# Optimization experiments

Measured on AMD Instinct MI355X. Metric: run time of the kernel, lower is better.

Reference implementation:

```python
import jax, jax.numpy as jnp
import numpy as np

N_NODES = 20000
N_EDGES = 320000
N_GRAPHS = 200
N_LAYERS = 2
TOWERS = 5
F_IN = 75        # divide_input=False -> each tower sees the full 75-dim input
F_OUT = 15       # out_channels // towers = 75 // 5
EDGE_DIM = 50
POST_IN = (4 * 3 + 1) * F_IN  # 4 aggregators * 3 scalers + self = 975
EPS_STD = 1e-5
EPS_BN = 1e-5


def setup_inputs() -> dict:
    key = jax.random.key(0)
    ks = jax.random.split(key, 16)
    x_idx = jax.random.randint(ks[0], (N_NODES,), 0, 10000)
    edge_index = jax.random.randint(ks[1], (2, N_EDGES), 0, N_NODES)
    edge_attr_idx = jax.random.randint(ks[2], (N_EDGES,), 0, 100)
    batch_idx = jnp.sort(jax.random.randint(ks[3], (N_NODES,), 0, N_GRAPHS))

    def g(k, shp, fan):
        return jax.random.normal(k, shp, jnp.float32) * np.float32(1.0 / np.sqrt(fan))

    inp = dict(
        x_idx=x_idx, edge_index=edge_index, edge_attr_idx=edge_attr_idx, batch_idx=batch_idx,
        node_emb=g(ks[4], (10000, F_IN), 1.0),
        edge_emb=g(ks[5], (100, EDGE_DIM), 1.0),
        W_edge=g(ks[6], (N_LAYERS, EDGE_DIM, F_IN), EDGE_DIM),
        b_edge=jnp.zeros((N_LAYERS, F_IN), jnp.float32),
        W_pre=g(ks[7], (N_LAYERS, TOWERS, 3 * F_IN, F_IN), 3 * F_IN),
        b_pre=jnp.zeros((N_LAYERS, TOWERS, F_IN), jnp.float32),
        W_post=g(ks[8], (N_LAYERS, TOWERS, POST_IN, F_OUT), POST_IN),
        b_post=jnp.zeros((N_LAYERS, TOWERS, F_OUT), jnp.float32),
        W_lin=g(ks[9], (N_LAYERS, F_IN, F_IN), F_IN),
        b_lin=jnp.zeros((N_LAYERS, F_IN), jnp.float32),
        bn_gamma=jnp.ones((N_LAYERS, F_IN), jnp.float32),
        bn_beta=jnp.zeros((N_LAYERS, F_IN), jnp.float32),
        W1=g(ks[10], (75, 50), 75), b1=jnp.zeros((50,), jnp.float32),
        W2=g(ks[11], (50, 25), 50), b2=jnp.zeros((25,), jnp.float32),
        W3=g(ks[12], (25, 1), 25), b3=jnp.zeros((1,), jnp.float32),
    )
    return inp


def reference(x_idx, edge_index, edge_attr_idx, batch_idx,
              node_emb, edge_emb, W_edge, b_edge, W_pre, b_pre,
              W_post, b_post, W_lin, b_lin, bn_gamma, bn_beta,
              W1, b1, W2, b2, W3, b3):
    src, dst = edge_index[0], edge_index[1]  # flow source_to_target: aggregate at dst
    x = node_emb[x_idx]                      # [N, 75]
    e_raw = edge_emb[edge_attr_idx]          # [E, 50]

    # in-degree based scalers (PNA); avg log-degree from this graph's degree histogram
    deg = jax.ops.segment_sum(jnp.ones((N_EDGES,), jnp.float32), dst, num_segments=N_NODES)
    avg_log = jnp.mean(jnp.log(deg + 1.0))
    deg_c = jnp.maximum(deg, 1.0)
    amp = (jnp.log(deg_c + 1.0) / avg_log)[:, None, None]
    att = (avg_log / jnp.log(deg_c + 1.0))[:, None, None]
    has_in = (deg > 0.0)[:, None, None]
    inv_deg = (1.0 / deg_c)[:, None, None]

    for l in range(N_LAYERS):
        # edge encoder (shared across towers)
        e = e_raw @ W_edge[l] + b_edge[l]                            # [E, 75]
        # message: since divide_input=False all towers see the same concat input
        h = jnp.concatenate([x[dst], x[src], e], axis=-1)            # [E, 225]
        m = jnp.einsum('ec,tcf->etf', h, W_pre[l]) + b_pre[l]        # [E, T, 75]
        # multi-aggregator reduction at dst
        mean = jax.ops.segment_sum(m, dst, num_segments=N_NODES) * inv_deg
        mean_sq = jax.ops.segment_sum(m * m, dst, num_segments=N_NODES) * inv_deg
        std = jnp.sqrt(jax.nn.relu(mean_sq - mean * mean) + EPS_STD)
        mn = jnp.where(has_in, jax.ops.segment_min(m, dst, num_segments=N_NODES), 0.0)
        mx = jnp.where(has_in, jax.ops.segment_max(m, dst, num_segments=N_NODES), 0.0)
        aggr = jnp.concatenate([mean, mn, mx, std], axis=-1)         # [N, T, 300]
        # degree scalers: identity, amplification, attenuation
        out = jnp.concatenate([aggr, aggr * amp, aggr * att], axis=-1)  # [N, T, 900]
        # update: concat self features, per-tower post MLP, then shared lin
        xt = jnp.broadcast_to(x[:, None, :], (N_NODES, TOWERS, F_IN))
        h2 = jnp.concatenate([xt, out], axis=-1)                     # [N, T, 975]
        y = jnp.einsum('ntc,tcf->ntf', h2, W_post[l]) + b_post[l]    # [N, T, 15]
        y = y.reshape(N_NODES, TOWERS * F_OUT) @ W_lin[l] + b_lin[l] # [N, 75]
        # BatchNorm (training-mode batch stats, biased variance) + ReLU
        mu = jnp.mean(y, axis=0)
        var = jnp.mean((y - mu) ** 2, axis=0)
        y = (y - mu) * jax.lax.rsqrt(var + EPS_BN) * bn_gamma[l] + bn_beta[l]
        x = jax.nn.relu(y)

    pooled = jax.ops.segment_sum(x, batch_idx, num_segments=N_GRAPHS)  # [G, 75]
    h = jax.nn.relu(pooled @ W1 + b1)
    h = jax.nn.relu(h @ W2 + b2)
    return h @ W3 + b3                                               # [G, 1]
```

## Files before the change

kernel.cpp:

```cpp
#include <hip/hip_runtime.h>
#include <hip/hip_bf16.h>
#include <math.h>

#define NN 20000
#define NE 320000
#define NG 200
#define FI 75
#define NT 5
#define FO 15
#define CH 375
#define PI 975
#define SMS 1608

typedef __attribute__((ext_vector_type(8))) short v8s;
typedef __attribute__((ext_vector_type(4))) float v4f;

__device__ __forceinline__ unsigned short f2bfu(float v) {
  __hip_bfloat16 h = __float2bfloat16(v);
  return *reinterpret_cast<unsigned short*>(&h);
}
__device__ __forceinline__ float uif(unsigned u) { return __uint_as_float(u); }

__global__ __launch_bounds__(256) void k_mega1(
    const int* __restrict__ xidx, const float* __restrict__ emb, float* __restrict__ x,
    const int* __restrict__ dstp, int* __restrict__ deg,
    const float* __restrict__ eemb, const float* __restrict__ W_edge,
    const float* __restrict__ b_edge, float* __restrict__ te,
    const float* __restrict__ W_pre, float* __restrict__ WAs,
    const float* __restrict__ W_post, float* __restrict__ V,
    const float* __restrict__ b_post, const float* __restrict__ W_lin,
    const float* __restrict__ b_lin, float* __restrict__ bc) {
  __shared__ float S[FI * 16];
  int b = blockIdx.x, tid = threadIdx.x;
  if (b < 5860) {
    int i = b * 256 + tid;
    if (i < NN * FI) {
      int n = i / FI, f = i - n * FI;
      x[i] = emb[xidx[n] * FI + f];
    }
  } else if (b < 7110) {
    int e = (b - 5860) * 256 + tid;
    if (e < NE) atomicAdd(&deg[dstp[e]], 1);
  } else if (b < 7310) {
    int la = b - 7110;
    int l = la / 100, a = la - l * 100;
    int f = tid;
    if (f < FI) {
      float acc = b_edge[l * FI + f];
      for (int j = 0; j < 50; ++j)
        acc = fmaf(eemb[a * 50 + j], W_edge[(l * 50 + j) * FI + f], acc);
      te[la * FI + f] = acc;
    }
  } else if (b < 7530) {
    int i = (b - 7310) * 256 + tid;
    if (i < 2 * FI * CH) {
      int c = i % CH;
      int k = (i / CH) % FI;
      int l = i / (CH * FI);
      int t = c / FI, f = c - t * FI;
      WAs[i] = W_pre[((size_t)(l * NT + t) * 225 + FI + k) * FI + f];
    }
  } else if (b < 7560) {
    int bid = b - 7530;
    int g = bid % 3;
    int lt = bid / 3;
    for (int idx = tid; idx < FI * 16; idx += 256) {
      int q = idx >> 4, f = idx & 15;
      float v = 0.f;
      if (f < FO) {
        const float* wb = W_post + (size_t)lt * PI * FO;
        int rowb = FI + g * 300 + q;
        v = wb[rowb * FO + f] + wb[(rowb + FI) * FO + f] + wb[(rowb + 2 * FI) * FO + f];
      }
      S[idx] = v;
    }
    __syncthreads();
    for (int idx = tid; idx < FI * 16; idx += 256) {
      int j = idx >> 4, f = idx & 15;
      float acc = 0.f;
      const float* wr = W_pre + ((size_t)lt * 225 + j) * FI;
      for (int q = 0; q < FI; ++q) acc = fmaf(wr[q], S[q * 16 + f], acc);
      V[((size_t)bid * FI + j) * 16 + f] = acc;
    }
  } else {
    int l = b - 7560;
    int g = tid;
    if (g < FI) {
      float acc = b_lin[l * FI + g];
      for (int j = 0; j < FI; ++j)
        acc = fmaf(b_post[l * FI + j], W_lin[(l * FI + j) * FI + g], acc);
      bc[l * 76 + g] = acc;
    }
  }
}

__global__ __launch_bounds__(1024) void k_mega2(
    const int* __restrict__ deg, int* __restrict__ off, int* __restrict__ cur,
    float* __restrict__ avglog,
    const float* __restrict__ te, const float* __restrict__ W_pre,
    const float* __restrict__ b_pre, unsigned short* __restrict__ tm,
    const float* __restrict__ W_post, const float* __restrict__ V,
    unsigned short* __restrict__ Bp,
    const float* __restrict__ WAs, unsigned short* __restrict__ Bxs,
    const float* __restrict__ W_lin, unsigned short* __restrict__ Blin) {
  __shared__ float red[1024];
  int b = blockIdx.x, t = threadIdx.x;
  if (b == 0) {
    int* wsum = (int*)red;
    int base = t * 20;
    int loc[20];
    int s = 0;
#pragma unroll
    for (int j = 0; j < 20; ++j) {
      int i = base + j;
      int v = (i < NN) ? deg[i] : 0;
      loc[j] = s;
      s += v;
    }
    int lane = t & 63, w = t >> 6;
    int inc = s;
    for (int o = 1; o < 64; o <<= 1) {
      int u = __shfl_up(inc, o, 64);
      if (lane >= o) inc += u;
    }
    if (lane == 63) wsum[w] = inc;
    __syncthreads();
    if (t == 0) {
      int a = 0;
#pragma unroll
      for (int k = 0; k < 16; ++k) { int v = wsum[k]; wsum[k] = a; a += v; }
    }
    __syncthreads();
    int tex = wsum[w] + inc - s;
#pragma unroll
    for (int j = 0; j < 20; ++j) {
      int i = base + j;
      if (i < NN) { int e = tex + loc[j]; off[i] = e; cur[i] = e; }
    }
    if (t == 1023) off[NN] = tex + s;
  } else if (b == 1) {
    float s = 0.f;
    for (int i = t; i < NN; i += 1024) s += logf((float)deg[i] + 1.f);
    red[t] = s;
    __syncthreads();
    for (int o = 512; o > 0; o >>= 1) {
      if (t < o) red[t] += red[t + o];
      __syncthreads();
    }
    if (t == 0) avglog[0] = red[0] / (float)NN;
  } else if (b < 77) {
    int idx = (b - 2) * 1024 + t;
    if (idx < 76800) {
      int la = idx / 384, c = idx - la * 384;
      int l = la / 100;
      float acc = 0.f;
      if (c < CH) {
        int tt = c / FI, f = c - tt * FI;
        acc = b_pre[(l * NT + tt) * FI + f];
        const float* ter = te + la * FI;
        for (int k = 0; k < FI; ++k)
          acc = fmaf(ter[k], W_pre[((size_t)(l * NT + tt) * 225 + 150 + k) * FI + f], acc);
      }
      tm[(size_t)la * 384 + c] = f2bfu(acc);
    }
  } else if (b < 302) {
    int i = (b - 77) * 1024 + t;
    if (i < 230400) {
      int j = i & 7;
      int lane = (i >> 3) & 63;
      int rem = i >> 9;
      int kb = rem % 15; rem /= 15;
      int g = rem % 3; rem /= 3;
      int tt = rem % 5;
      int l = rem / 5;
      int k = kb * 32 + (lane >> 4) * 8 + j;
      int f = lane & 15;
      float w = 0.f;
      if (f < FO) {
        int lt = l * NT + tt;
        if (k < 300) {
          int a = k / 75, ch = k - a * 75;
          w = W_post[((size_t)lt * PI + FI + g * 300 + a * 75 + ch) * FO + f];
        } else if (k >= 320 && k < 395) {
          w = V[(((size_t)(lt * 3 + g)) * FI + (k - 320)) * 16 + f];
        } else if (k >= 395 && k < 470 && g == 0) {
          w = W_post[((size_t)lt * PI + (k - 395)) * FO + f];
        }
      }
      Bp[i] = f2bfu(w);
    }
  } else if (b < 374) {
    int i = (b - 302) * 1024 + t;
    if (i < 73728) {
      int j = i & 7;
      int lane = (i >> 3) & 63;
      int rem = i >> 9;
      int nt = rem % 24; rem /= 24;
      int kb = rem % 3;
      int l = rem / 3;
      int k = kb * 32 + (lane >> 4) * 8 + j;
      int n = nt * 16 + (lane & 15);
      float w = 0.f;
      if (k < FI && n < CH) w = WAs[(size_t)l * FI * CH + k * CH + n];
      Bxs[i] = f2bfu(w);
    }
  } else {
    int i = (b - 374) * 1024 + t;
    if (i < 15360) {
      int j = i & 7;
      int lane = (i >> 3) & 63;
      int rem = i >> 9;
      int nt = rem % 5; rem /= 5;
      int kb = rem % 3;
      int l = rem / 3;
      int k = kb * 32 + (lane >> 4) * 8 + j;
      int f = nt * 16 + (lane & 15);
      float w = 0.f;
      if (k < FI && f < FI) w = W_lin[(size_t)l * FI * FI + k * FI + f];
      Blin[i] = f2bfu(w);
    }
  }
}

__global__ __launch_bounds__(256) void k_mega3(
    const int* __restrict__ srcp, const int* __restrict__ dstp,
    const int* __restrict__ attr, int* __restrict__ cur, int2* __restrict__ csr,
    const int* __restrict__ deg, const float* __restrict__ avglog,
    float* __restrict__ amp, float* __restrict__ att, float* __restrict__ inv) {
  int b = blockIdx.x, t = threadIdx.x;
  if (b < 1250) {
    int e = b * 256 + t;
    if (e < NE) {
      int pos = atomicAdd(&cur[dstp[e]], 1);
      csr[pos] = make_int2(srcp[e], attr[e]);
    }
  } else {
    int i = (b - 1250) * 256 + t;
    if (i < NN) {
      float dc = fmaxf((float)deg[i], 1.f);
      float ld = logf(dc + 1.f);
      float av = avglog[0];
      amp[i] = ld / av;
      att[i] = av / ld;
      inv[i] = 1.f / dc;
    }
  }
}

__global__ __launch_bounds__(256) void k_gemm_xs(const float* __restrict__ x,
                                                 const unsigned short* __restrict__ BxsL,
                                                 unsigned short* __restrict__ xsb,
                                                 const int* __restrict__ deg,
                                                 unsigned short* __restrict__ xh,
                                                 float* __restrict__ bnsum) {
  int tid = threadIdx.x;
  if (blockIdx.y == 1) {
    if (blockIdx.x == 0 && tid < 150) bnsum[tid] = 0.f;
    for (int i = blockIdx.x * 256 + tid; i < NN * 160; i += 625 * 256) {
      int r = i / 160, k = i - r * 160;
      float v = 0.f;
      if (k < FI) v = x[(size_t)r * FI + k] * ((deg[r] > 0) ? 1.f : 0.f);
      else if (k < 150) v = x[(size_t)r * FI + k - FI];
      xh[i] = f2bfu(v);
    }
    return;
  }
  __shared__ unsigned short As[32 * 104];
  __shared__ unsigned short Os[32 * 384];
  int m0 = blockIdx.x * 32;
  for (int i = tid; i < 32 * 104; i += 256) {
    int r = i / 104, k = i - r * 104;
    As[i] = (k < FI) ? f2bfu(x[(size_t)(m0 + r) * FI + k]) : 0;
  }
  __syncthreads();
  int lane = tid & 63, w = tid >> 6;
  int m16 = lane & 15, quad = lane >> 4;
  v4f acc0[6], acc1[6];
#pragma unroll
  for (int nt = 0; nt < 6; ++nt) {
    acc0[nt] = {0.f, 0.f, 0.f, 0.f};
    acc1[nt] = {0.f, 0.f, 0.f, 0.f};
  }
  const unsigned short* arow0 = As + m16 * 104 + quad * 8;
  const unsigned short* arow1 = As + (16 + m16) * 104 + quad * 8;
#pragma unroll
  for (int kb = 0; kb < 3; ++kb) {
    v8s a0 = *(const v8s*)(arow0 + kb * 32);
    v8s a1 = *(const v8s*)(arow1 + kb * 32);
#pragma unroll
    for (int nt = 0; nt < 6; ++nt) {
      v8s bf = *(const v8s*)(BxsL + ((size_t)(kb * 24 + w * 6 + nt) * 64 + lane) * 8);
      acc0[nt] = __builtin_amdgcn_mfma_f32_16x16x32_bf16(a0, bf, acc0[nt], 0, 0, 0);
      acc1[nt] = __builtin_amdgcn_mfma_f32_16x16x32_bf16(a1, bf, acc1[nt], 0, 0, 0);
    }
  }
#pragma unroll
  for (int nt = 0; nt < 6; ++nt) {
    int col = w * 96 + nt * 16 + m16;
#pragma unroll
    for (int r = 0; r < 4; ++r) {
      Os[(quad * 4 + r) * 384 + col] = f2bfu(acc0[nt][r]);
      Os[(16 + quad * 4 + r) * 384 + col] = f2bfu(acc1[nt][r]);
    }
  }
  __syncthreads();
  uint4* dst = (uint4*)(xsb + (size_t)m0 * 384);
  const uint4* src = (const uint4*)Os;
  for (int i = tid; i < 1536; i += 256) dst[i] = src[i];
}

__global__ __launch_bounds__(1024) void k_aggpost(
    const unsigned short* __restrict__ xs, const int2* __restrict__ csr,
    const int* __restrict__ off, const float* __restrict__ inv_deg,
    const unsigned short* __restrict__ tm, const unsigned short* __restrict__ xh,
    const unsigned short* __restrict__ Bp, const float* __restrict__ amp,
    const float* __restrict__ att, const unsigned short* __restrict__ BlinL,
    const float* __restrict__ bcL, float* __restrict__ yout,
    float* __restrict__ bnsum) {
  __shared__ __align__(16) unsigned short sm[16 * SMS];
  __shared__ __align__(16) unsigned short zs[16 * 96];
  __shared__ float ysum[FI], ysq[FI];
  int tid = threadIdx.x;
  int wv = tid >> 6, lane = tid & 63;
  int rel0 = blockIdx.x * 16;
  int n = rel0 + wv;
  if (tid < FI) { ysum[tid] = 0.f; ysq[tid] = 0.f; }
  for (int idx = tid; idx < 1600; idx += 1024) {
    int h = idx / 100, pp = idx - h * 100;
    int t = pp / 20, cc = pp - t * 20;
    sm[h * SMS + t * 320 + 300 + cc] = 0;
  }
  for (int i = tid; i < 16 * 21; i += 1024) {
    int r = i / 21, k = 75 + i - r * 21;
    zs[r * 96 + k] = 0;
  }
  if (n < NN) {
    int c0 = lane * 6;
    int o0 = off[n], o1 = off[n + 1];
    float s[6], q[6], mn[6], mx[6];
#pragma unroll
    for (int j = 0; j < 6; ++j) {
      s[j] = 0.f; q[j] = 0.f; mn[j] = INFINITY; mx[j] = -INFINITY;
    }
    auto proc = [&](uint3 xv, uint3 tv) {
      unsigned xa[3] = {xv.x, xv.y, xv.z};
      unsigned ta[3] = {tv.x, tv.y, tv.z};
#pragma unroll
      for (int j = 0; j < 3; ++j) {
        float z0 = uif(xa[j] << 16) + uif(ta[j] << 16);
        float z1 = uif(xa[j] & 0xffff0000u) + uif(ta[j] & 0xffff0000u);
        s[2 * j] += z0; q[2 * j] = fmaf(z0, z0, q[2 * j]);
        mn[2 * j] = fminf(mn[2 * j], z0); mx[2 * j] = fmaxf(mx[2 * j], z0);
        s[2 * j + 1] += z1; q[2 * j + 1] = fmaf(z1, z1, q[2 * j + 1]);
        mn[2 * j + 1] = fminf(mn[2 * j + 1], z1); mx[2 * j + 1] = fmaxf(mx[2 * j + 1], z1);
      }
    };
    int i = o0;
    for (; i + 4 <= o1; i += 4) {
      int2 e0 = csr[i], e1 = csr[i + 1], e2 = csr[i + 2], e3 = csr[i + 3];
      uint3 x0 = *(const uint3*)(xs + (size_t)e0.x * 384 + c0);
      uint3 t0 = *(const uint3*)(tm + (size_t)e0.y * 384 + c0);
      uint3 x1 = *(const uint3*)(xs + (size_t)e1.x * 384 + c0);
      uint3 t1 = *(const uint3*)(tm + (size_t)e1.y * 384 + c0);
      uint3 x2 = *(const uint3*)(xs + (size_t)e2.x * 384 + c0);
      uint3 t2 = *(const uint3*)(tm + (size_t)e2.y * 384 + c0);
      uint3 x3 = *(const uint3*)(xs + (size_t)e3.x * 384 + c0);
      uint3 t3 = *(const uint3*)(tm + (size_t)e3.y * 384 + c0);
      proc(x0, t0); proc(x1, t1); proc(x2, t2); proc(x3, t3);
    }
    for (; i < o1; ++i) {
      int2 e0 = csr[i];
      uint3 x0 = *(const uint3*)(xs + (size_t)e0.x * 384 + c0);
      uint3 t0 = *(const uint3*)(tm + (size_t)e0.y * 384 + c0);
      proc(x0, t0);
    }
    float inv = inv_deg[n];
    bool empty = (o1 == o0);
    unsigned short* srow = sm + wv * SMS;
#pragma unroll
    for (int j = 0; j < 6; ++j) {
      int c = c0 + j;
      if (c < CH) {
        float me = s[j] * inv;
        float sd = sqrtf(fmaxf(q[j] * inv - me * me, 0.f) + 1e-5f);
        float mnv = empty ? 0.f : mn[j];
        float mxv = empty ? 0.f : mx[j];
        int t = c / 75, ch = c - t * 75;
        unsigned short* bb = srow + t * 320;
        bb[ch] = f2bfu(me);
        bb[75 + ch] = f2bfu(mnv);
        bb[150 + ch] = f2bfu(mxv);
        bb[225 + ch] = f2bfu(sd);
      }
    }
  } else {
    uint* rowz = (uint*)(sm + wv * SMS);
    for (int idx2 = lane; idx2 < SMS / 2; idx2 += 64) rowz[idx2] = 0;
  }
  __syncthreads();
  int m16 = lane & 15, quad = lane >> 4;
  if (wv < NT) {
    int tw = wv;
    const unsigned short* arow = sm + m16 * SMS + tw * 320 + quad * 8;
    const unsigned short* xrow = xh + (size_t)(rel0 + m16) * 160 + quad * 8;
    const unsigned short* bp = Bp + ((size_t)tw * 3 * 15 * 64) * 8 + lane * 8;
    v4f a0 = {0.f, 0.f, 0.f, 0.f}, a1 = a0, a2 = a0;
#pragma unroll
    for (int kb = 0; kb < 15; ++kb) {
      v8s av = *(const v8s*)((kb < 10) ? (arow + kb * 32) : (xrow + (kb - 10) * 32));
      const unsigned short* bb = bp + (size_t)kb * 512;
      v8s b0 = *(const v8s*)(bb);
      v8s b1 = *(const v8s*)(bb + 15 * 512);
      v8s b2 = *(const v8s*)(bb + 30 * 512);
      a0 = __builtin_amdgcn_mfma_f32_16x16x32_bf16(av, b0, a0, 0, 0, 0);
      a1 = __builtin_amdgcn_mfma_f32_16x16x32_bf16(av, b1, a1, 0, 0, 0);
      a2 = __builtin_amdgcn_mfma_f32_16x16x32_bf16(av, b2, a2, 0, 0, 0);
    }
    int f = m16;
    if (f < FO) {
      int relZ = quad * 4;
#pragma unroll
      for (int r = 0; r < 4; ++r) {
        int nd = rel0 + relZ + r;
        int ndc = (nd < NN) ? nd : (NN - 1);
        float zz = a0[r] + amp[ndc] * a1[r] + att[ndc] * a2[r];
        zs[(relZ + r) * 96 + tw * FO + f] = f2bfu(zz);
      }
    }
  }
  __syncthreads();
  if (wv < NT) {
    int tw = wv;
    v4f acc2 = {0.f, 0.f, 0.f, 0.f};
#pragma unroll
    for (int kb = 0; kb < 3; ++kb) {
      v8s av = *(const v8s*)(zs + m16 * 96 + quad * 8 + kb * 32);
      v8s bl = *(const v8s*)(BlinL + ((size_t)(kb * 5 + tw) * 64 + lane) * 8);
      acc2 = __builtin_amdgcn_mfma_f32_16x16x32_bf16(av, bl, acc2, 0, 0, 0);
    }
    int fcol = tw * 16 + m16;
    if (fcol < FI) {
      float bcf = bcL[fcol];
      int nb = rel0 + quad * 4;
#pragma unroll
      for (int r = 0; r < 4; ++r) {
        int nd = nb + r;
        if (nd < NN) {
          float v = acc2[r] + bcf;
          yout[(size_t)nd * FI + fcol] = v;
          atomicAdd(&ysum[fcol], v);
          atomicAdd(&ysq[fcol], v * v);
        }
      }
    }
  }
  __syncthreads();
  if (tid < FI) {
    atomicAdd(&bnsum[tid], ysum[tid]);
    atomicAdd(&bnsum[FI + tid], ysq[tid]);
  }
}

__global__ __launch_bounds__(256) void k_bnfinapply(const float* __restrict__ y,
    const float* __restrict__ bnsum, const float* __restrict__ gamL,
    const float* __restrict__ betL, float* __restrict__ xo,
    const int* __restrict__ batch, float* __restrict__ pooled, int dopool) {
  __shared__ float sc[150];
  int tid = threadIdx.x;
  if (tid < FI) {
    float mu = bnsum[tid] / (float)NN;
    float var = bnsum[FI + tid] / (float)NN - mu * mu;
    float scl = gamL[tid] * rsqrtf(var + 1e-5f);
    sc[tid] = scl;
    sc[FI + tid] = betL[tid] - mu * scl;
  }
  if (!dopool) {
    for (int i = blockIdx.x * 256 + tid; i < NG * FI; i += gridDim.x * 256)
      pooled[i] = 0.f;
  }
  __syncthreads();
  int stride = gridDim.x * 256;
  for (int i = blockIdx.x * 256 + tid; i < NN * FI; i += stride) {
    int n = i / FI, f = i - n * FI;
    float v = fmaxf(fmaf(y[i], sc[f], sc[FI + f]), 0.f);
    xo[i] = v;
    if (dopool) atomicAdd(&pooled[batch[n] * FI + f], v);
  }
}

__global__ void k_head(const float* __restrict__ pooled, const float* __restrict__ W1,
                       const float* __restrict__ b1, const float* __restrict__ W2,
                       const float* __restrict__ b2, const float* __restrict__ W3,
                       const float* __restrict__ b3, float* __restrict__ out) {
  __shared__ float p[FI], h1[50], h2[25];
  int g = blockIdx.x, t = threadIdx.x;
  for (int i = t; i < FI; i += 64) p[i] = pooled[g * FI + i];
  __syncthreads();
  if (t < 50) {
    float a = b1[t];
    for (int j = 0; j < FI; ++j) a = fmaf(p[j], W1[j * 50 + t], a);
    h1[t] = fmaxf(a, 0.f);
  }
  __syncthreads();
  if (t < 25) {
    float a = b2[t];
    for (int j = 0; j < 50; ++j) a = fmaf(h1[j], W2[j * 25 + t], a);
    h2[t] = fmaxf(a, 0.f);
  }
  __syncthreads();
  if (t == 0) {
    float a = b3[0];
    for (int j = 0; j < 25; ++j) a = fmaf(h2[j], W3[j], a);
    out[g] = a;
  }
}

extern "C" void kernel_launch(void* const* d_in, const int* in_sizes, int n_in,
                              void* d_out, int out_size, void* d_ws, size_t ws_size,
                              hipStream_t stream) {
  const int* x_idx = (const int*)d_in[0];
  const int* eidx  = (const int*)d_in[1];
  const int* srcp  = eidx;
  const int* dstp  = eidx + NE;
  const int* eattr = (const int*)d_in[2];
  const int* batch = (const int*)d_in[3];
  const float* node_emb = (const float*)d_in[4];
  const float* edge_emb = (const float*)d_in[5];
  const float* W_edge = (const float*)d_in[6];
  const float* b_edge = (const float*)d_in[7];
  const float* W_pre  = (const float*)d_in[8];
  const float* b_pre  = (const float*)d_in[9];
  const float* W_post = (const float*)d_in[10];
  const float* b_post = (const float*)d_in[11];
  const float* W_lin  = (const float*)d_in[12];
  const float* b_lin  = (const float*)d_in[13];
  const float* gam = (const float*)d_in[14];
  const float* bet = (const float*)d_in[15];
  const float* W1 = (const float*)d_in[16];
  const float* b1 = (const float*)d_in[17];
  const float* W2 = (const float*)d_in[18];
  const float* b2 = (const float*)d_in[19];
  const float* W3 = (const float*)d_in[20];
  const float* b3 = (const float*)d_in[21];

  char* p = (char*)d_ws;
  auto alloc = [&](size_t b) -> char* {
    char* r = p;
    p += (b + 255) & ~(size_t)255;
    return r;
  };
  float* x_a   = (float*)alloc((size_t)NN * FI * 4);
  float* x_b   = (float*)alloc((size_t)NN * FI * 4);
  unsigned short* xs_bf = (unsigned short*)alloc((size_t)NN * 384 * 2);
  float* z     = (float*)alloc((size_t)NN * FI * 4);
  unsigned short* xh = (unsigned short*)alloc((size_t)(NN + 64) * 160 * 2);
  float* te    = (float*)alloc(2 * 100 * FI * 4);
  unsigned short* tm_bf = (unsigned short*)alloc((size_t)2 * 100 * 384 * 2);
  float* WAs   = (float*)alloc((size_t)2 * FI * CH * 4);
  float* V     = (float*)alloc((size_t)2 * NT * 3 * FI * 16 * 4);
  unsigned short* Bpk = (unsigned short*)alloc((size_t)230400 * 2);
  unsigned short* Bxs = (unsigned short*)alloc((size_t)73728 * 2);
  unsigned short* Blin = (unsigned short*)alloc((size_t)15360 * 2);
  float* bc    = (float*)alloc(2 * 76 * 4);
  float* ampv  = (float*)alloc((size_t)NN * 4);
  float* attv  = (float*)alloc((size_t)NN * 4);
  float* invv  = (float*)alloc((size_t)NN * 4);
  float* avglog = (float*)alloc(256);
  float* bnsum = (float*)alloc(2 * FI * 4);
  float* pooled = (float*)alloc((size_t)NG * FI * 4);
  int* deg = (int*)alloc((size_t)NN * 4);
  int* off = (int*)alloc((size_t)(NN + 1) * 4);
  int* cur = (int*)alloc((size_t)NN * 4);
  int2* csr = (int2*)alloc((size_t)NE * 8);

  hipMemsetAsync(deg, 0, (size_t)NN * 4, stream);

  k_mega1<<<7562, 256, 0, stream>>>(x_idx, node_emb, x_a, dstp, deg,
                                    edge_emb, W_edge, b_edge, te,
                                    W_pre, WAs, W_post, V,
                                    b_post, W_lin, b_lin, bc);
  k_mega2<<<389, 1024, 0, stream>>>(deg, off, cur, avglog,
                                    te, W_pre, b_pre, tm_bf, W_post, V, Bpk,
                                    WAs, Bxs, W_lin, Blin);
  k_mega3<<<1329, 256, 0, stream>>>(srcp, dstp, eattr, cur, csr,
                                    deg, avglog, ampv, attv, invv);

  for (int l = 0; l < 2; ++l) {
    const float* xin = (l == 0) ? x_a : x_b;
    float* xout = (l == 0) ? x_b : x_a;
    k_gemm_xs<<<dim3(625, 2), 256, 0, stream>>>(xin, Bxs + (size_t)l * 36864,
                                                xs_bf, deg, xh, bnsum);
    k_aggpost<<<1250, 1024, 0, stream>>>(xs_bf, csr, off, invv,
                                         tm_bf + (size_t)l * 100 * 384, xh,
                                         Bpk + (size_t)l * 115200, ampv, attv,
                                         Blin + (size_t)l * 7680, bc + l * 76,
                                         z, bnsum);
    k_bnfinapply<<<1250, 256, 0, stream>>>(z, bnsum, gam + l * FI, bet + l * FI,
                                           xout, batch, pooled, (l == 1) ? 1 : 0);
  }

  k_head<<<NG, 64, 0, stream>>>(pooled, W1, b1, W2, b2, W3, b3, (float*)d_out);
}
```

Measured before the change: 433.1 us.

## Compute per-edge pre-MLP messages via MFMA inside aggregation instead of per-node precompute

Drops the per-node x·W_pre GEMM kernel and the precomputed per-edge-type term table. The aggregation kernel now gathers raw bf16 source features and edge-embedding rows into shared memory for each 32-edge tile, using a warp-specialized, double-buffered staging loop. It then runs MFMA over a stacked [x | te] K=160 weight to form the messages before reducing mean/min/max/std. This reads 160 bf16 per edge instead of 750 and removes one kernel, at the cost of more MFMA work per edge and a sync per tile.

```diff
diff --git a/kernel.cpp b/kernel.cpp
--- a/kernel.cpp
+++ b/kernel.cpp
@@ -97,11 +97,11 @@
 __global__ __launch_bounds__(1024) void k_mega2(
     const int* __restrict__ deg, int* __restrict__ off, int* __restrict__ cur,
     float* __restrict__ avglog,
-    const float* __restrict__ te, const float* __restrict__ W_pre,
-    const float* __restrict__ b_pre, unsigned short* __restrict__ tm,
+    const float* __restrict__ te, unsigned short* __restrict__ tq,
+    const float* __restrict__ W_pre,
     const float* __restrict__ W_post, const float* __restrict__ V,
     unsigned short* __restrict__ Bp,
-    const float* __restrict__ WAs, unsigned short* __restrict__ Bxs,
+    const float* __restrict__ WAs, unsigned short* __restrict__ Bx2,
     const float* __restrict__ W_lin, unsigned short* __restrict__ Blin) {
   __shared__ float red[1024];
   int b = blockIdx.x, t = threadIdx.x;
@@ -148,23 +148,36 @@
       __syncthreads();
     }
     if (t == 0) avglog[0] = red[0] / (float)NN;
-  } else if (b < 77) {
+  } else if (b < 18) {
     int idx = (b - 2) * 1024 + t;
-    if (idx < 76800) {
-      int la = idx / 384, c = idx - la * 384;
-      int l = la / 100;
-      float acc = 0.f;
-      if (c < CH) {
-        int tt = c / FI, f = c - tt * FI;
-        acc = b_pre[(l * NT + tt) * FI + f];
-        const float* ter = te + la * FI;
-        for (int k = 0; k < FI; ++k)
-          acc = fmaf(ter[k], W_pre[((size_t)(l * NT + tt) * 225 + 150 + k) * FI + f], acc);
+    if (idx < 16000) {
+      int la = idx / 80, k = idx - la * 80;
+      tq[idx] = (k < FI) ? f2bfu(te[la * FI + k]) : 0;
+    }
+  } else if (b < 138) {
+    int i = (b - 18) * 1024 + t;
+    if (i < 122880) {
+      int j = i & 7;
+      int lane = (i >> 3) & 63;
+      int rem = i >> 9;
+      int nt = rem % 24; rem /= 24;
+      int kb = rem % 5;
+      int l = rem / 5;
+      int k = kb * 32 + (lane >> 4) * 8 + j;
+      int n = nt * 16 + (lane & 15);
+      float w = 0.f;
+      if (n < CH) {
+        if (k < FI) {
+          w = WAs[(size_t)l * FI * CH + k * CH + n];
+        } else if (k >= 80 && k < 80 + FI) {
+          int tt = n / 75, f = n - tt * 75;
+          w = W_pre[((size_t)(l * NT + tt) * 225 + 150 + (k - 80)) * FI + f];
+        }
       }
-      tm[(size_t)la * 384 + c] = f2bfu(acc);
-    }
-  } else if (b < 302) {
-    int i = (b - 77) * 1024 + t;
+      Bx2[i] = f2bfu(w);
+    }
+  } else if (b < 363) {
+    int i = (b - 138) * 1024 + t;
     if (i < 230400) {
       int j = i & 7;
       int lane = (i >> 3) & 63;
@@ -189,23 +202,8 @@
       }
       Bp[i] = f2bfu(w);
     }
-  } else if (b < 374) {
-    int i = (b - 302) * 1024 + t;
-    if (i < 73728) {
-      int j = i & 7;
-      int lane = (i >> 3) & 63;
-      int rem = i >> 9;
-      int nt = rem % 24; rem /= 24;
-      int kb = rem % 3;
-      int l = rem / 3;
-      int k = kb * 32 + (lane >> 4) * 8 + j;
-      int n = nt * 16 + (lane & 15);
-      float w = 0.f;
-      if (k < FI && n < CH) w = WAs[(size_t)l * FI * CH + k * CH + n];
-      Bxs[i] = f2bfu(w);
-    }
   } else {
-    int i = (b - 374) * 1024 + t;
+    int i = (b - 363) * 1024 + t;
     if (i < 15360) {
       int j = i & 7;
       int lane = (i >> 3) & 63;
@@ -247,83 +245,46 @@
   }
 }
 
-__global__ __launch_bounds__(256) void k_gemm_xs(const float* __restrict__ x,
-                                                 const unsigned short* __restrict__ BxsL,
-                                                 unsigned short* __restrict__ xsb,
-                                                 const int* __restrict__ deg,
-                                                 unsigned short* __restrict__ xh,
-                                                 float* __restrict__ bnsum) {
+__global__ __launch_bounds__(256) void k_prepx(const float* __restrict__ x,
+                                               const int* __restrict__ deg,
+                                               unsigned short* __restrict__ xh,
+                                               unsigned short* __restrict__ xq,
+                                               float* __restrict__ bnsum) {
   int tid = threadIdx.x;
-  if (blockIdx.y == 1) {
-    if (blockIdx.x == 0 && tid < 150) bnsum[tid] = 0.f;
-    for (int i = blockIdx.x * 256 + tid; i < NN * 160; i += 625 * 256) {
-      int r = i / 160, k = i - r * 160;
-      float v = 0.f;
-      if (k < FI) v = x[(size_t)r * FI + k] * ((deg[r] > 0) ? 1.f : 0.f);
-      else if (k < 150) v = x[(size_t)r * FI + k - FI];
-      xh[i] = f2bfu(v);
-    }
-    return;
-  }
-  __shared__ unsigned short As[32 * 104];
-  __shared__ unsigned short Os[32 * 384];
-  int m0 = blockIdx.x * 32;
-  for (int i = tid; i < 32 * 104; i += 256) {
-    int r = i / 104, k = i - r * 104;
-    As[i] = (k < FI) ? f2bfu(x[(size_t)(m0 + r) * FI + k]) : 0;
-  }
-  __syncthreads();
-  int lane = tid & 63, w = tid >> 6;
-  int m16 = lane & 15, quad = lane >> 4;
-  v4f acc0[6], acc1[6];
-#pragma unroll
-  for (int nt = 0; nt < 6; ++nt) {
-    acc0[nt] = {0.f, 0.f, 0.f, 0.f};
-    acc1[nt] = {0.f, 0.f, 0.f, 0.f};
-  }
-  const unsigned short* arow0 = As + m16 * 104 + quad * 8;
-  const unsigned short* arow1 = As + (16 + m16) * 104 + quad * 8;
-#pragma unroll
-  for (int kb = 0; kb < 3; ++kb) {
-    v8s a0 = *(const v8s*)(arow0 + kb * 32);
-    v8s a1 = *(const v8s*)(arow1 + kb * 32);
-#pragma unroll
-    for (int nt = 0; nt < 6; ++nt) {
-      v8s bf = *(const v8s*)(BxsL + ((size_t)(kb * 24 + w * 6 + nt) * 64 + lane) * 8);
-      acc0[nt] = __builtin_amdgcn_mfma_f32_16x16x32_bf16(a0, bf, acc0[nt], 0, 0, 0);
-      acc1[nt] = __builtin_amdgcn_mfma_f32_16x16x32_bf16(a1, bf, acc1[nt], 0, 0, 0);
-    }
-  }
-#pragma unroll
-  for (int nt = 0; nt < 6; ++nt) {
-    int col = w * 96 + nt * 16 + m16;
-#pragma unroll
-    for (int r = 0; r < 4; ++r) {
-      Os[(quad * 4 + r) * 384 + col] = f2bfu(acc0[nt][r]);
-      Os[(16 + quad * 4 + r) * 384 + col] = f2bfu(acc1[nt][r]);
-    }
-  }
-  __syncthreads();
-  uint4* dst = (uint4*)(xsb + (size_t)m0 * 384);
-  const uint4* src = (const uint4*)Os;
-  for (int i = tid; i < 1536; i += 256) dst[i] = src[i];
+  if (blockIdx.x == 0 && tid < 150) bnsum[tid] = 0.f;
+  for (int i = blockIdx.x * 256 + tid; i < NN * 160; i += 625 * 256) {
+    int r = i / 160, k = i - r * 160;
+    float v = 0.f;
+    if (k < FI) v = x[(size_t)r * FI + k] * ((deg[r] > 0) ? 1.f : 0.f);
+    else if (k < 150) v = x[(size_t)r * FI + k - FI];
+    xh[i] = f2bfu(v);
+  }
+  for (int i = blockIdx.x * 256 + tid; i < NN * 80; i += 625 * 256) {
+    int r = i / 80, k = i - r * 80;
+    xq[i] = (k < FI) ? f2bfu(x[(size_t)r * FI + k]) : 0;
+  }
 }
 
 __global__ __launch_bounds__(1024) void k_aggpost(
-    const unsigned short* __restrict__ xs, const int2* __restrict__ csr,
-    const int* __restrict__ off, const float* __restrict__ inv_deg,
-    const unsigned short* __restrict__ tm, const unsigned short* __restrict__ xh,
+    const unsigned short* __restrict__ xq, const unsigned short* __restrict__ tqL,
+    const int2* __restrict__ csr, const int* __restrict__ off,
+    const float* __restrict__ inv_deg, const unsigned short* __restrict__ xh,
     const unsigned short* __restrict__ Bp, const float* __restrict__ amp,
     const float* __restrict__ att, const unsigned short* __restrict__ BlinL,
-    const float* __restrict__ bcL, float* __restrict__ yout,
-    float* __restrict__ bnsum) {
+    const float* __restrict__ bcL, const float* __restrict__ bpreL,
+    float* __restrict__ yout, float* __restrict__ bnsum,
+    const unsigned short* __restrict__ Bx2L) {
   __shared__ __align__(16) unsigned short sm[16 * SMS];
+  __shared__ __align__(16) unsigned short Ab[2][32 * 168];
   __shared__ __align__(16) unsigned short zs[16 * 96];
+  __shared__ int offL[17];
+  __shared__ int cumR[17];
   __shared__ float ysum[FI], ysq[FI];
   int tid = threadIdx.x;
   int wv = tid >> 6, lane = tid & 63;
+  int m16 = lane & 15, quad = lane >> 4;
   int rel0 = blockIdx.x * 16;
-  int n = rel0 + wv;
+  if (tid < 17) offL[tid] = off[rel0 + tid];
   if (tid < FI) { ysum[tid] = 0.f; ysq[tid] = 0.f; }
   for (int idx = tid; idx < 1600; idx += 1024) {
     int h = idx / 100, pp = idx - h * 100;
@@ -334,71 +295,165 @@
     int r = i / 21, k = 75 + i - r * 21;
     zs[r * 96 + k] = 0;
   }
-  if (n < NN) {
-    int c0 = lane * 6;
-    int o0 = off[n], o1 = off[n + 1];
-    float s[6], q[6], mn[6], mx[6];
-#pragma unroll
-    for (int j = 0; j < 6; ++j) {
-      s[j] = 0.f; q[j] = 0.f; mn[j] = INFINITY; mx[j] = -INFINITY;
-    }
-    auto proc = [&](uint3 xv, uint3 tv) {
-      unsigned xa[3] = {xv.x, xv.y, xv.z};
-      unsigned ta[3] = {tv.x, tv.y, tv.z};
-#pragma unroll
-      for (int j = 0; j < 3; ++j) {
-        float z0 = uif(xa[j] << 16) + uif(ta[j] << 16);
-        float z1 = uif(xa[j] & 0xffff0000u) + uif(ta[j] & 0xffff0000u);
-        s[2 * j] += z0; q[2 * j] = fmaf(z0, z0, q[2 * j]);
-        mn[2 * j] = fminf(mn[2 * j], z0); mx[2 * j] = fmaxf(mx[2 * j], z0);
-        s[2 * j + 1] += z1; q[2 * j + 1] = fmaf(z1, z1, q[2 * j + 1]);
-        mn[2 * j + 1] = fminf(mn[2 * j + 1], z1); mx[2 * j + 1] = fmaxf(mx[2 * j + 1], z1);
+  __syncthreads();
+  if (tid == 0) {
+    int a = 0;
+#pragma unroll
+    for (int i = 0; i < 16; ++i) {
+      cumR[i] = a;
+      a += (offL[i + 1] - offL[i] + 31) >> 5;
+    }
+    cumR[16] = a;
+  }
+  int nt0 = 2 * wv;
+  int col0 = nt0 * 16 + m16, col1 = col0 + 16;
+  v8s B00, B01, B02, B03, B04, B10, B11, B12, B13, B14;
+  float cb0 = 0.f, cb1 = 0.f;
+  float s0 = 0.f, q0 = 0.f, mn0 = INFINITY, mx0 = -INFINITY;
+  float s1 = 0.f, q1 = 0.f, mn1 = INFINITY, mx1 = -INFINITY;
+  if (wv < 12) {
+    B00 = *(const v8s*)(Bx2L + ((size_t)(0 * 24 + nt0) * 64 + lane) * 8);
+    B01 = *(const v8s*)(Bx2L + ((size_t)(1 * 24 + nt0) * 64 + lane) * 8);
+    B02 = *(const v8s*)(Bx2L + ((size_t)(2 * 24 + nt0) * 64 + lane) * 8);
+    B03 = *(const v8s*)(Bx2L + ((size_t)(3 * 24 + nt0) * 64 + lane) * 8);
+    B04 = *(const v8s*)(Bx2L + ((size_t)(4 * 24 + nt0) * 64 + lane) * 8);
+    B10 = *(const v8s*)(Bx2L + ((size_t)(0 * 24 + nt0 + 1) * 64 + lane) * 8);
+    B11 = *(const v8s*)(Bx2L + ((size_t)(1 * 24 + nt0 + 1) * 64 + lane) * 8);
+    B12 = *(const v8s*)(Bx2L + ((size_t)(2 * 24 + nt0 + 1) * 64 + lane) * 8);
+    B13 = *(const v8s*)(Bx2L + ((size_t)(3 * 24 + nt0 + 1) * 64 + lane) * 8);
+    B14 = *(const v8s*)(Bx2L + ((size_t)(4 * 24 + nt0 + 1) * 64 + lane) * 8);
+    if (col0 < CH) cb0 = bpreL[col0];
+    if (col1 < CH) cb1 = bpreL[col1];
+    float sd0 = sqrtf(1e-5f);
+    for (int i = 0; i < 16; ++i) {
+      if (offL[i + 1] == offL[i] && quad == 0) {
+#pragma unroll
+        for (int h = 0; h < 2; ++h) {
+          int col = h ? col1 : col0;
+          if (col < CH) {
+            int tc = col / 75, ch = col - tc * 75;
+            unsigned short* bb = sm + i * SMS + tc * 320;
+            bb[ch] = 0; bb[75 + ch] = 0; bb[150 + ch] = 0; bb[225 + ch] = f2bfu(sd0);
+          }
+        }
       }
-    };
-    int i = o0;
-    for (; i + 4 <= o1; i += 4) {
-      int2 e0 = csr[i], e1 = csr[i + 1], e2 = csr[i + 2], e3 = csr[i + 3];
-      uint3 x0 = *(const uint3*)(xs + (size_t)e0.x * 384 + c0);
-      uint3 t0 = *(const uint3*)(tm + (size_t)e0.y * 384 + c0);
-      uint3 x1 = *(const uint3*)(xs + (size_t)e1.x * 384 + c0);
-      uint3 t1 = *(const uint3*)(tm + (size_t)e1.y * 384 + c0);
-      uint3 x2 = *(const uint3*)(xs + (size_t)e2.x * 384 + c0);
-      uint3 t2 = *(const uint3*)(tm + (size_t)e2.y * 384 + c0);
-      uint3 x3 = *(const uint3*)(xs + (size_t)e3.x * 384 + c0);
-      uint3 t3 = *(const uint3*)(tm + (size_t)e3.y * 384 + c0);
-      proc(x0, t0); proc(x1, t1); proc(x2, t2); proc(x3, t3);
-    }
-    for (; i < o1; ++i) {
-      int2 e0 = csr[i];
-      uint3 x0 = *(const uint3*)(xs + (size_t)e0.x * 384 + c0);
-      uint3 t0 = *(const uint3*)(tm + (size_t)e0.y * 384 + c0);
-      proc(x0, t0);
-    }
-    float inv = inv_deg[n];
-    bool empty = (o1 == o0);
-    unsigned short* srow = sm + wv * SMS;
-#pragma unroll
-    for (int j = 0; j < 6; ++j) {
-      int c = c0 + j;
-      if (c < CH) {
-        float me = s[j] * inv;
-        float sd = sqrtf(fmaxf(q[j] * inv - me * me, 0.f) + 1e-5f);
-        float mnv = empty ? 0.f : mn[j];
-        float mxv = empty ? 0.f : mx[j];
-        int t = c / 75, ch = c - t * 75;
-        unsigned short* bb = srow + t * 320;
-        bb[ch] = f2bfu(me);
-        bb[75 + ch] = f2bfu(mnv);
-        bb[150 + ch] = f2bfu(mxv);
-        bb[225 + ch] = f2bfu(sd);
+    }
+  }
+  __syncthreads();
+  int R = cumR[16];
+  int t2 = tid - 768;
+  int E0 = t2 / 20, C0 = t2 - E0 * 20;
+  int E1 = (t2 + 256) / 20, C1 = (t2 + 256) - E1 * 20;
+  int E2 = (t2 + 512) / 20, C2 = (t2 + 512) - E2 * 20;
+  int2 cs0 = make_int2(0, 0), cs1 = cs0, cs2 = cs0;
+  int siS = 0;
+  const uint4* xq4 = (const uint4*)xq;
+  const uint4* tq4 = (const uint4*)tqL;
+  uint4* Ab4 = (uint4*)Ab;
+  auto prefetchCsr = [&](int Y) {
+    while (Y >= cumR[siS + 1]) ++siS;
+    int bs = offL[siS] + (Y - cumR[siS]) * 32;
+    int om = offL[siS + 1] - 1;
+    int e0 = bs + E0; if (e0 > om) e0 = om;
+    int e1 = bs + E1; if (e1 > om) e1 = om;
+    cs0 = csr[e0];
+    cs1 = csr[e1];
+    if (t2 < 128) { int e2 = bs + E2; if (e2 > om) e2 = om; cs2 = csr[e2]; }
+  };
+  auto stageWrite = [&](int X) {
+    uint4* dst = Ab4 + (X & 1) * 672;
+    dst[E0 * 21 + C0] = (C0 < 10) ? xq4[(size_t)cs0.x * 10 + C0]
+                                  : tq4[(size_t)cs0.y * 10 + (C0 - 10)];
+    dst[E1 * 21 + C1] = (C1 < 10) ? xq4[(size_t)cs1.x * 10 + C1]
+                                  : tq4[(size_t)cs1.y * 10 + (C1 - 10)];
+    if (t2 < 128)
+      dst[E2 * 21 + C2] = (C2 < 10) ? xq4[(size_t)cs2.x * 10 + C2]
+                                    : tq4[(size_t)cs2.y * 10 + (C2 - 10)];
+  };
+  auto subtile = [&](const unsigned short* A, int base, int o1m1) {
+    const unsigned short* ar = A + m16 * 168 + quad * 8;
+    v8s a0 = *(const v8s*)(ar);
+    v8s a1 = *(const v8s*)(ar + 32);
+    v8s a2 = *(const v8s*)(ar + 64);
+    v8s a3 = *(const v8s*)(ar + 96);
+    v8s a4 = *(const v8s*)(ar + 128);
+    v4f p0 = {0.f, 0.f, 0.f, 0.f}, p1 = p0;
+    p0 = __builtin_amdgcn_mfma_f32_16x16x32_bf16(a0, B00, p0, 0, 0, 0);
+    p0 = __builtin_amdgcn_mfma_f32_16x16x32_bf16(a1, B01, p0, 0, 0, 0);
+    p0 = __builtin_amdgcn_mfma_f32_16x16x32_bf16(a2, B02, p0, 0, 0, 0);
+    p0 = __builtin_amdgcn_mfma_f32_16x16x32_bf16(a3, B03, p0, 0, 0, 0);
+    p0 = __builtin_amdgcn_mfma_f32_16x16x32_bf16(a4, B04, p0, 0, 0, 0);
+    p1 = __builtin_amdgcn_mfma_f32_16x16x32_bf16(a0, B10, p1, 0, 0, 0);
+    p1 = __builtin_amdgcn_mfma_f32_16x16x32_bf16(a1, B11, p1, 0, 0, 0);
+    p1 = __builtin_amdgcn_mfma_f32_16x16x32_bf16(a2, B12, p1, 0, 0, 0);
+    p1 = __builtin_amdgcn_mfma_f32_16x16x32_bf16(a3, B13, p1, 0, 0, 0);
+    p1 = __builtin_amdgcn_mfma_f32_16x16x32_bf16(a4, B14, p1, 0, 0, 0);
+    int er = base + quad * 4;
+#pragma unroll
+    for (int j = 0; j < 4; ++j) {
+      bool v = (er + j) <= o1m1;
+      float z = p0[j] + cb0;
+      s0 = v ? s0 + z : s0;
+      q0 = v ? fmaf(z, z, q0) : q0;
+      mn0 = v ? fminf(mn0, z) : mn0;
+      mx0 = v ? fmaxf(mx0, z) : mx0;
+      float w = p1[j] + cb1;
+      s1 = v ? s1 + w : s1;
+      q1 = v ? fmaf(w, w, q1) : q1;
+      mn1 = v ? fminf(mn1, w) : mn1;
+      mx1 = v ? fmaxf(mx1, w) : mx1;
+    }
+  };
+  if (wv >= 12 && R > 0) {
+    prefetchCsr(0);
+    stageWrite(0);
+    if (R > 1) prefetchCsr(1);
+  }
+  __syncthreads();
+  int ci = 0;
+  for (int r = 0; r < R; ++r) {
+    if (wv >= 12) {
+      if (r + 1 < R) stageWrite(r + 1);
+      if (r + 2 < R) prefetchCsr(r + 2);
+    } else {
+      while (r >= cumR[ci + 1]) ++ci;
+      int o0i = offL[ci], o1i = offL[ci + 1];
+      int base = o0i + (r - cumR[ci]) * 32;
+      const unsigned short* A = (const unsigned short*)Ab + (r & 1) * (32 * 168);
+      int o1m1 = o1i - 1;
+      subtile(A, base, o1m1);
+      if (base + 16 < o1i) subtile(A + 16 * 168, base + 16, o1m1);
+      if (r == cumR[ci + 1] - 1) {
+        float inv = inv_deg[rel0 + ci];
+#pragma unroll
+        for (int h = 0; h < 2; ++h) {
+          float S = h ? s1 : s0, Q = h ? q1 : q0;
+          float MN = h ? mn1 : mn0, MX = h ? mx1 : mx0;
+          S += __shfl_xor(S, 16); S += __shfl_xor(S, 32);
+          Q += __shfl_xor(Q, 16); Q += __shfl_xor(Q, 32);
+          MN = fminf(MN, __shfl_xor(MN, 16)); MN = fminf(MN, __shfl_xor(MN, 32));
+          MX = fmaxf(MX, __shfl_xor(MX, 16)); MX = fmaxf(MX, __shfl_xor(MX, 32));
+          if (quad == 0) {
+            int col = h ? col1 : col0;
+            if (col < CH) {
+              float me = S * inv;
+              float sd = sqrtf(fmaxf(Q * inv - me * me, 0.f) + 1e-5f);
+              int tc = col / 75, ch = col - tc * 75;
+              unsigned short* bb = sm + ci * SMS + tc * 320;
+              bb[ch] = f2bfu(me);
+              bb[75 + ch] = f2bfu(MN);
+              bb[150 + ch] = f2bfu(MX);
+              bb[225 + ch] = f2bfu(sd);
+            }
+          }
+        }
+        s0 = 0.f; q0 = 0.f; mn0 = INFINITY; mx0 = -INFINITY;
+        s1 = 0.f; q1 = 0.f; mn1 = INFINITY; mx1 = -INFINITY;
       }
     }
-  } else {
-    uint* rowz = (uint*)(sm + wv * SMS);
-    for (int idx2 = lane; idx2 < SMS / 2; idx2 += 64) rowz[idx2] = 0;
-  }
-  __syncthreads();
-  int m16 = lane & 15, quad = lane >> 4;
+    __syncthreads();
+  }
+  __syncthreads();
   if (wv < NT) {
     int tw = wv;
     const unsigned short* arow = sm + m16 * SMS + tw * 320 + quad * 8;
@@ -551,15 +606,15 @@
   };
   float* x_a   = (float*)alloc((size_t)NN * FI * 4);
   float* x_b   = (float*)alloc((size_t)NN * FI * 4);
-  unsigned short* xs_bf = (unsigned short*)alloc((size_t)NN * 384 * 2);
+  unsigned short* xq = (unsigned short*)alloc((size_t)NN * 80 * 2);
   float* z     = (float*)alloc((size_t)NN * FI * 4);
   unsigned short* xh = (unsigned short*)alloc((size_t)(NN + 64) * 160 * 2);
   float* te    = (float*)alloc(2 * 100 * FI * 4);
-  unsigned short* tm_bf = (unsigned short*)alloc((size_t)2 * 100 * 384 * 2);
+  unsigned short* tq = (unsigned short*)alloc((size_t)2 * 100 * 80 * 2);
   float* WAs   = (float*)alloc((size_t)2 * FI * CH * 4);
   float* V     = (float*)alloc((size_t)2 * NT * 3 * FI * 16 * 4);
   unsigned short* Bpk = (unsigned short*)alloc((size_t)230400 * 2);
-  unsigned short* Bxs = (unsigned short*)alloc((size_t)73728 * 2);
+  unsigned short* Bx2 = (unsigned short*)alloc((size_t)122880 * 2);
   unsigned short* Blin = (unsigned short*)alloc((size_t)15360 * 2);
   float* bc    = (float*)alloc(2 * 76 * 4);
   float* ampv  = (float*)alloc((size_t)NN * 4);
@@ -579,22 +634,21 @@
                                     edge_emb, W_edge, b_edge, te,
                                     W_pre, WAs, W_post, V,
                                     b_post, W_lin, b_lin, bc);
-  k_mega2<<<389, 1024, 0, stream>>>(deg, off, cur, avglog,
-                                    te, W_pre, b_pre, tm_bf, W_post, V, Bpk,
-                                    WAs, Bxs, W_lin, Blin);
+  k_mega2<<<378, 1024, 0, stream>>>(deg, off, cur, avglog,
+                                    te, tq, W_pre, W_post, V, Bpk,
+                                    WAs, Bx2, W_lin, Blin);
   k_mega3<<<1329, 256, 0, stream>>>(srcp, dstp, eattr, cur, csr,
                                     deg, avglog, ampv, attv, invv);
 
   for (int l = 0; l < 2; ++l) {
     const float* xin = (l == 0) ? x_a : x_b;
     float* xout = (l == 0) ? x_b : x_a;
-    k_gemm_xs<<<dim3(625, 2), 256, 0, stream>>>(xin, Bxs + (size_t)l * 36864,
-                                                xs_bf, deg, xh, bnsum);
-    k_aggpost<<<1250, 1024, 0, stream>>>(xs_bf, csr, off, invv,
-                                         tm_bf + (size_t)l * 100 * 384, xh,
-                                         Bpk + (size_t)l * 115200, ampv, attv,
+    k_prepx<<<625, 256, 0, stream>>>(xin, deg, xh, xq, bnsum);
+    k_aggpost<<<1250, 1024, 0, stream>>>(xq, tq + (size_t)l * 8000, csr, off, invv,
+                                         xh, Bpk + (size_t)l * 115200, ampv, attv,
                                          Blin + (size_t)l * 7680, bc + l * 76,
-                                         z, bnsum);
+                                         b_pre + (size_t)l * CH,
+                                         z, bnsum, Bx2 + (size_t)l * 61440);
     k_bnfinapply<<<1250, 256, 0, stream>>>(z, bnsum, gam + l * FI, bet + l * FI,
                                            xout, batch, pooled, (l == 1) ? 1 : 0);
   }
```

Result: slower. 679.4 us (+56.9%).
